# Kernel optimization log

Measured on AMD Instinct MI355X. Metric: run time of the kernel, lower is better.

## Reference

```python
import jax, jax.numpy as jnp
from jax import lax
import numpy as np

B, A, C = 8, 49104, 90
IMG = 512.0            # 512 + compound_coef*128, coef=0
SCORE_THR = 0.2
IOU_THR = 0.2
K_PRE = 1000           # top candidates kept before NMS (standard TF-style padded NMS)
K_OUT = 100            # max detections per image


def setup_inputs() -> dict:
    key = jax.random.key(0)
    k1, k2, k3, k4, k5, k6 = jax.random.split(key, 6)
    cls_preds = jax.random.uniform(k1, (B, A, C), dtype=jnp.float32)
    loc_preds = 0.1 * jax.random.normal(k2, (B, A, 4), dtype=jnp.float32)
    # plausible anchors in (y1, x1, y2, x2) within the 512x512 image
    cy = jax.random.uniform(k3, (A,)) * IMG
    cx = jax.random.uniform(k4, (A,)) * IMG
    h = 16.0 + jax.random.uniform(k5, (A,)) * 112.0
    w = 16.0 + jax.random.uniform(k6, (A,)) * 112.0
    anchors = jnp.stack([cy - h / 2, cx - w / 2, cy + h / 2, cx + w / 2], axis=-1).astype(jnp.float32)
    return {"cls_preds": cls_preds, "loc_preds": loc_preds, "anchors": anchors}


def _decode_and_clip(anchors, loc_preds):
    # anchors: [A,4] (y1,x1,y2,x2); loc_preds: [B,A,4] (dy,dx,dh,dw)
    ya = (anchors[:, 0] + anchors[:, 2]) / 2
    xa = (anchors[:, 1] + anchors[:, 3]) / 2
    ha = anchors[:, 2] - anchors[:, 0]
    wa = anchors[:, 3] - anchors[:, 1]
    dy, dx, dh, dw = loc_preds[..., 0], loc_preds[..., 1], loc_preds[..., 2], loc_preds[..., 3]
    h = jnp.exp(dh) * ha
    w = jnp.exp(dw) * wa
    yc = dy * ha + ya
    xc = dx * wa + xa
    # output boxes in (xmin, ymin, xmax, ymax), clipped to image
    boxes = jnp.stack([xc - w / 2, yc - h / 2, xc + w / 2, yc + h / 2], axis=-1)
    return jnp.clip(boxes, 0.0, IMG)


def _pairwise_iou(boxes):
    # boxes: [K,4] xyxy -> [K,K]
    x1 = jnp.maximum(boxes[:, None, 0], boxes[None, :, 0])
    y1 = jnp.maximum(boxes[:, None, 1], boxes[None, :, 1])
    x2 = jnp.minimum(boxes[:, None, 2], boxes[None, :, 2])
    y2 = jnp.minimum(boxes[:, None, 3], boxes[None, :, 3])
    inter = jnp.clip(x2 - x1, 0.0) * jnp.clip(y2 - y1, 0.0)
    area = (boxes[:, 2] - boxes[:, 0]) * (boxes[:, 3] - boxes[:, 1])
    return inter / (area[:, None] + area[None, :] - inter + 1e-8)


def _nms_single(scores, classes, boxes):
    # scores: [A], classes: [A] int32, boxes: [A,4]
    masked = jnp.where(scores > SCORE_THR, scores, -1.0)
    vals, idx = lax.top_k(masked, K_PRE)          # top candidates
    b = boxes[idx]                                 # [K_PRE,4]
    cls = classes[idx]                             # [K_PRE]
    # batched_nms trick: offset boxes per class so cross-class IoU is 0
    off = b + cls[:, None].astype(b.dtype) * (IMG + 1.0)
    ious = _pairwise_iou(off)                      # [K_PRE,K_PRE]

    def body(keep, i):
        sup = jnp.any(keep & (ious[:, i] > IOU_THR))
        k = (vals[i] > SCORE_THR) & (~sup)
        return keep.at[i].set(k), None

    keep, _ = lax.scan(body, jnp.zeros((K_PRE,), bool), jnp.arange(K_PRE))
    final = jnp.where(keep, vals, -1.0)
    fvals, fidx = lax.top_k(final, K_OUT)
    det = fvals > 0.0
    out_boxes = jnp.where(det[:, None], b[fidx], jnp.array([0.0, 0.0, 1.0, 1.0], dtype=b.dtype))
    out_scores = jnp.where(det, fvals, 0.0)
    out_labels = jnp.where(det, cls[fidx], -1)
    return out_boxes, out_scores, out_labels


def reference(cls_preds, loc_preds, anchors):
    boxes = _decode_and_clip(anchors, loc_preds)   # [B,A,4]
    scores = jnp.max(cls_preds, axis=2)            # [B,A]
    classes = jnp.argmax(cls_preds, axis=2).astype(jnp.int32)
    out_boxes, out_scores, out_labels = jax.vmap(_nms_single)(scores, classes, boxes)
    return out_boxes, out_scores, out_labels
```

## Files before the change

### kernel.cpp

```cpp
#include <hip/hip_runtime.h>
#include <stdint.h>

#define B_    8
#define A_    49104
#define C_    90
#define IMG_  512.0f
#define THR_  0.2f
#define KPRE  1000
#define KOUT  100
#define NCAND 1024
#define NKEY  2048
#define NBIN  1024
#define BINBASE 0x17C99u
#define THRU    0xBE4CCCCDu
#define GANCH 64
#define PREF_F 0.9997f

#define NPAD 1088
#define PADI(j) ((j) + ((j) >> 4))

static __device__ __forceinline__ uint32_t f2ord(float f) {
    uint32_t b = __float_as_uint(f);
    return (b & 0x80000000u) ? ~b : (b | 0x80000000u);
}
static __device__ __forceinline__ float ord2f(uint32_t u) {
    uint32_t b = (u & 0x80000000u) ? (u & 0x7FFFFFFFu) : ~u;
    return __uint_as_float(b);
}

__global__ __launch_bounds__(256)
void k_score_compact(const float* __restrict__ cls,
                     uint32_t* __restrict__ scores_u,
                     uint64_t* __restrict__ keybuf,
                     uint32_t* __restrict__ cntg) {
    __shared__ float4 s4[(GANCH * C_) / 4];
    __shared__ float r_val[GANCH];
    __shared__ int   r_cls[GANCH];

    int tid = threadIdx.x;
    int b = blockIdx.y;
    int a0 = blockIdx.x * GANCH;
    int valid = A_ - a0; if (valid > GANCH) valid = GANCH;

    const float4* src = (const float4*)(cls + (size_t)(b * A_ + a0) * C_);
    if (valid == GANCH) {
        float4 v0 = src[tid];
        float4 v1 = src[tid + 256];
        float4 v2 = src[tid + 512];
        float4 v3 = src[tid + 768];
        float4 v4 = src[tid + 1024];
        float4 v5;
        if (tid < 160) v5 = src[tid + 1280];
        s4[tid]        = v0;
        s4[tid + 256]  = v1;
        s4[tid + 512]  = v2;
        s4[tid + 768]  = v3;
        s4[tid + 1024] = v4;
        if (tid < 160) s4[tid + 1280] = v5;
    } else {
        int n4 = (valid * C_) / 4;
        for (int i = tid; i < n4; i += 256) s4[i] = src[i];
    }
    __syncthreads();

    const float* s = (const float*)s4;
    int g = tid >> 2, sub = tid & 3;
    float best = -1.0f; int bi = 0;
    if (g < valid) {
        #pragma unroll
        for (int j = sub; j < C_ + 2; j += 4) {
            if (j < C_) {
                float v = s[g * C_ + j];
                if (v > best) { best = v; bi = j; }
            }
        }
    }
    #pragma unroll
    for (int d = 1; d < 4; d <<= 1) {
        float ov = __shfl_xor(best, d);
        int   oi = __shfl_xor(bi, d);
        if (ov > best || (ov == best && oi < bi)) { best = ov; bi = oi; }
    }
    if (sub == 0 && g < valid) { r_val[g] = best; r_cls[g] = bi; }
    __syncthreads();

    if (tid < 64) {
        int a = a0 + tid;
        bool v = tid < valid;
        float bv = v ? r_val[tid] : -1.0f;
        if (v) {
            float m = (bv > THR_) ? bv : -1.0f;
            scores_u[b * A_ + a] = f2ord(m);
        }
        bool flag = v && (bv >= PREF_F);
        unsigned long long mb = __ballot(flag);
        if (mb) {
            uint32_t base = 0;
            if (tid == 0) base = atomicAdd(&cntg[b], (uint32_t)__popcll(mb));
            base = (uint32_t)__shfl((int)base, 0);
            if (flag) {
                int p = (int)base + (int)__popcll(mb & ((1ull << tid) - 1ull));
                if (p < NKEY) {
                    uint64_t key = ((uint64_t)f2ord(bv) << 32)
                                 | ((uint64_t)((~(uint32_t)a) & 0xFFFFu) << 16)
                                 | ((uint64_t)(uint32_t)r_cls[tid] << 8);
                    keybuf[b * NKEY + p] = key;
                }
            }
        }
    }
}

__global__ __launch_bounds__(1024)
void k_seltop2(const uint32_t* __restrict__ scores_u,
               const float* __restrict__ cls,
               const float* __restrict__ loc,
               const float* __restrict__ anc,
               const uint64_t* __restrict__ keybuf,
               const uint32_t* __restrict__ cntg,
               float* __restrict__ cand_val,
               int* __restrict__ cand_cls,
               float* __restrict__ cand_box,
               int* __restrict__ n_valid) {
    int b = blockIdx.x;
    int t = threadIdx.x;
    __shared__ uint64_t keys[NKEY];
    __shared__ uint32_t sh_coarse;
    __shared__ int      sh_rem;
    __shared__ uint32_t sh_cutoff;
    __shared__ int      sh_cnt;
    const uint32_t* su = scores_u + (size_t)b * A_;

    int n = (int)cntg[b];
    bool fast = (n >= KPRE && n <= NKEY);

    if (fast) {
        for (int i = t; i < NKEY; i += 1024)
            keys[i] = (i < n) ? keybuf[b * NKEY + i] : 0ull;
    } else {
        uint32_t* h = (uint32_t*)keys;
        h[t] = 0;
        if (t == 0) sh_cnt = 0;
        __syncthreads();
        for (int a = t; a < A_; a += 1024) {
            uint32_t u = su[a];
            if (u > THRU) {
                int bin = (int)(u >> 15) - (int)BINBASE;
                bin = bin < 0 ? 0 : (bin >= NBIN ? NBIN - 1 : bin);
                atomicAdd(&h[bin], 1u);
            }
        }
        __syncthreads();
        for (int d = 1; d < NBIN; d <<= 1) {
            uint32_t add = (t + d < NBIN) ? h[t + d] : 0u;
            __syncthreads();
            h[t] += add;
            __syncthreads();
        }
        {
            uint32_t St = h[t];
            uint32_t Sn = (t + 1 < NBIN) ? h[t + 1] : 0u;
            if (St >= KPRE && Sn < KPRE) {
                sh_coarse = (BINBASE + (uint32_t)t) << 15;
                sh_rem = KPRE - (int)Sn;
            }
            if (t == 0 && h[0] < KPRE) {
                sh_rem = 0;
                sh_coarse = 0xFFFFFFFFu;
                sh_cutoff = BINBASE << 15;
            }
        }
        __syncthreads();
        uint32_t coarse = sh_coarse;
        int rem = sh_rem;

        h[t] = 0;
        __syncthreads();
        if (rem > 0) {
            for (int a = t; a < A_; a += 1024) {
                uint32_t u = su[a];
                if ((u & 0xFFFF8000u) == coarse)
                    atomicAdd(&h[(u >> 5) & 0x3FF], 1u);
            }
        }
        __syncthreads();
        for (int d = 1; d < NBIN; d <<= 1) {
            uint32_t add = (t + d < NBIN) ? h[t + d] : 0u;
            __syncthreads();
            h[t] += add;
            __syncthreads();
        }
        if (rem > 0) {
            int St = (int)h[t];
            int Sn = (t + 1 < NBIN) ? (int)h[t + 1] : 0;
            if (St >= rem && Sn < rem)
                sh_cutoff = coarse | ((uint32_t)t << 5);
        }
        __syncthreads();
        uint32_t cutoff = sh_cutoff;
        __syncthreads();

        for (int a = t; a < A_; a += 1024) {
            uint32_t u = su[a];
            if (u >= cutoff) {
                int p = atomicAdd(&sh_cnt, 1);
                if (p < NKEY)
                    keys[p] = ((uint64_t)u << 32)
                            | ((uint64_t)((~(uint32_t)a) & 0xFFFFu) << 16);
            }
        }
        __syncthreads();
        n = sh_cnt; if (n > NKEY) n = NKEY;
        for (int i = t; i < NKEY; i += 1024)
            if (i >= n) keys[i] = 0ull;
    }
    __syncthreads();

    for (int kk = 2; kk <= NKEY; kk <<= 1) {
        for (int jj = kk >> 1; jj > 0; jj >>= 1) {
            int i1 = ((t & ~(jj - 1)) << 1) | (t & (jj - 1));
            int i2 = i1 + jj;
            uint64_t va = keys[i1], vb = keys[i2];
            bool desc = ((i1 & kk) == 0);
            if ((va < vb) == desc) { keys[i1] = vb; keys[i2] = va; }
            __syncthreads();
        }
    }

    uint64_t key = keys[t];
    bool real = (t < n);
    int ci = b * NCAND + t;
    if (real) {
        int a = (int)((~(uint32_t)(key >> 16)) & 0xFFFFu);
        int c;
        if (fast) {
            c = (int)((key >> 8) & 0xFFu);
        } else {
            const float* row = cls + ((size_t)b * A_ + a) * C_;
            float bb = -1.0f; int bc = 0;
            for (int j = 0; j < C_; ++j) { float q = row[j]; if (q > bb) { bb = q; bc = j; } }
            c = bc;
        }
        float4 an = ((const float4*)anc)[a];
        float4 l4 = ((const float4*)loc)[(size_t)b * A_ + a];
        float ya = (an.x + an.z) * 0.5f;
        float xa = (an.y + an.w) * 0.5f;
        float ha = an.z - an.x;
        float wa = an.w - an.y;
        float hh = expf(l4.z) * ha;
        float ww = expf(l4.w) * wa;
        float yc = l4.x * ha + ya;
        float xc = l4.y * wa + xa;
        float4 bx;
        bx.x = fminf(fmaxf(xc - ww * 0.5f, 0.0f), IMG_);
        bx.y = fminf(fmaxf(yc - hh * 0.5f, 0.0f), IMG_);
        bx.z = fminf(fmaxf(xc + ww * 0.5f, 0.0f), IMG_);
        bx.w = fminf(fmaxf(yc + hh * 0.5f, 0.0f), IMG_);
        cand_val[ci] = ord2f((uint32_t)(key >> 32));
        cand_cls[ci] = c;
        ((float4*)cand_box)[ci] = bx;
    } else {
        cand_val[ci] = -1.0f;
        cand_cls[ci] = 0;
        float4 z; z.x = z.y = z.z = z.w = 0.0f;
        ((float4*)cand_box)[ci] = z;
    }
    if (t == 0) n_valid[b] = n < KPRE ? n : KPRE;
}

__global__ void k_masks(const float* __restrict__ cand_box,
                        const int* __restrict__ cand_cls,
                        unsigned short* __restrict__ M16) {
    int b = blockIdx.x;
    __shared__ float x1s[NPAD], y1s[NPAD], x2s[NPAD], y2s[NPAD], ars[NPAD];
    for (int i = threadIdx.x; i < NCAND; i += blockDim.x) {
        int ci = b * NCAND + i;
        float4 bx = ((const float4*)cand_box)[ci];
        float off = (float)cand_cls[ci] * (IMG_ + 1.0f);
        float ox1 = bx.x + off, oy1 = bx.y + off;
        float ox2 = bx.z + off, oy2 = bx.w + off;
        int ip = PADI(i);
        x1s[ip] = ox1; y1s[ip] = oy1; x2s[ip] = ox2; y2s[ip] = oy2;
        ars[ip] = (ox2 - ox1) * (oy2 - oy1);
    }
    __syncthreads();

    int row0 = blockIdx.y * 63;
    for (int item = threadIdx.x; item < 63 * 64; item += blockDim.x) {
        int i = row0 + (item >> 6);
        if (i >= KPRE) continue;
        int w = item & 63;
        if (w < (i >> 4)) continue;
        int ip = PADI(i);
        float xi1 = x1s[ip], yi1 = y1s[ip], xi2 = x2s[ip], yi2 = y2s[ip], ai = ars[ip];
        unsigned int m = 0;
        int j0 = w * 16;
        #pragma unroll
        for (int q = 0; q < 16; ++q) {
            int jp = PADI(j0 + q);
            float xx1 = fmaxf(xi1, x1s[jp]);
            float yy1 = fmaxf(yi1, y1s[jp]);
            float xx2 = fminf(xi2, x2s[jp]);
            float yy2 = fminf(yi2, y2s[jp]);
            float iw = xx2 - xx1; iw = iw > 0.0f ? iw : 0.0f;
            float ih = yy2 - yy1; ih = ih > 0.0f ? ih : 0.0f;
            float inter = iw * ih;
            float den = (ai + ars[jp]) - inter + 1e-8f;
            float iou = inter / den;
            m |= (iou > THR_ ? 1u : 0u) << q;
        }
        M16[((size_t)(b * NCAND + i)) * 64 + w] = (unsigned short)m;
    }
}

__global__ void k_nms_out(const unsigned short* __restrict__ M16,
                          const float* __restrict__ cand_val,
                          const int* __restrict__ cand_cls,
                          const float* __restrict__ cand_box,
                          const int* __restrict__ n_valid,
                          float* __restrict__ out) {
    int b = blockIdx.x;
    int lane = threadIdx.x;
    int nv = n_valid[b]; if (nv > KPRE) nv = KPRE;
    const unsigned short* Mr = M16 + (size_t)b * NCAND * 64;
    __shared__ int kept[KOUT];

    uint32_t S = 0;
    int cnt = 0;
    uint32_t cur[8], nxt[8];
    #pragma unroll
    for (int t = 0; t < 8; ++t) cur[t] = Mr[(size_t)t * 64 + lane];

    for (int base = 0; base < nv && cnt < KOUT; base += 8) {
        #pragma unroll
        for (int t = 0; t < 8; ++t) {
            int r = base + 8 + t;
            nxt[t] = Mr[(size_t)(r < NCAND ? r : 0) * 64 + lane];
        }
        #pragma unroll
        for (int t = 0; t < 8; ++t) {
            int i = base + t;
            bool inb = (i < nv) && (cnt < KOUT);
            unsigned long long ball =
                __ballot(inb && (((S >> (i & 15)) & 1u) != 0u));
            int sup = (int)((ball >> (i >> 4)) & 1ull);
            if (inb && !sup) {
                S |= cur[t];
                if (lane == 0) kept[cnt] = i;
                cnt++;
            }
        }
        #pragma unroll
        for (int t = 0; t < 8; ++t) cur[t] = nxt[t];
    }
    __syncthreads();

    for (int s_ = lane; s_ < KOUT; s_ += 64) {
        float b0 = 0.0f, b1 = 0.0f, b2 = 1.0f, b3 = 1.0f, sc = 0.0f, lb = -1.0f;
        if (s_ < cnt) {
            int i = kept[s_];
            int ci = b * NCAND + i;
            float4 bx = ((const float4*)cand_box)[ci];
            b0 = bx.x; b1 = bx.y; b2 = bx.z; b3 = bx.w;
            sc = cand_val[ci];
            lb = (float)cand_cls[ci];
        }
        int ob = (b * KOUT + s_) * 4;
        out[ob + 0] = b0; out[ob + 1] = b1; out[ob + 2] = b2; out[ob + 3] = b3;
        out[B_ * KOUT * 4 + b * KOUT + s_] = sc;
        out[B_ * KOUT * 5 + b * KOUT + s_] = lb;
    }
}

extern "C" void kernel_launch(void* const* d_in, const int* in_sizes, int n_in,
                              void* d_out, int out_size, void* d_ws, size_t ws_size,
                              hipStream_t stream) {
    const float* cls = (const float*)d_in[0];
    const float* loc = (const float*)d_in[1];
    const float* anc = (const float*)d_in[2];
    float* out = (float*)d_out;

    char* ws = (char*)d_ws;
    size_t off = 0;
    auto alloc = [&](size_t bytes) -> void* {
        void* p = ws + off;
        off += (bytes + 255) & ~(size_t)255;
        return p;
    };
    uint32_t* scores_u = (uint32_t*)alloc((size_t)B_ * A_ * 4);
    uint64_t* keybuf   = (uint64_t*)alloc((size_t)B_ * NKEY * 8);
    uint32_t* cntg     = (uint32_t*)alloc((size_t)B_ * 4);
    float*    cand_val = (float*)   alloc((size_t)B_ * NCAND * 4);
    int*      cand_cls = (int*)     alloc((size_t)B_ * NCAND * 4);
    float*    cand_box = (float*)   alloc((size_t)B_ * NCAND * 4 * 4);
    int*      n_valid  = (int*)     alloc((size_t)B_ * 4);
    unsigned short* M16 = (unsigned short*)alloc((size_t)B_ * NCAND * 64 * 2);

    hipMemsetAsync(cntg, 0, (size_t)B_ * 4, stream);

    dim3 gD((A_ + GANCH - 1) / GANCH, B_);
    k_score_compact<<<gD, 256, 0, stream>>>(cls, scores_u, keybuf, cntg);
    k_seltop2<<<B_, 1024, 0, stream>>>(
        scores_u, cls, loc, anc, keybuf, cntg,
        cand_val, cand_cls, cand_box, n_valid);
    k_masks<<<dim3(B_, 16), 256, 0, stream>>>(cand_box, cand_cls, M16);
    k_nms_out<<<B_, 64, 0, stream>>>(
        M16, cand_val, cand_cls, cand_box, n_valid, out);
}
```

Before: 282.6 us.

## Replace global atomic compaction with per-block key slots and register bitonic sort

The score kernel no longer appends candidate keys to one global buffer through an atomic counter. Each block now writes its keys and count into its own slot, and the top-select kernel rebuilds a contiguous key array with a 1024-wide prefix scan. This removes the global atomics and the memset launch. The bitonic sort now keeps two keys per thread in registers, uses wavefront shuffles for strides below 64 and shared memory only for larger strides, so it needs fewer barriers. The cost is an extra prefix scan and serial per-block copy loops in the single-block-per-image kernel.

```diff
diff --git a/kernel.cpp b/kernel.cpp
--- a/kernel.cpp
+++ b/kernel.cpp
@@ -14,6 +14,7 @@
 #define BINBASE 0x17C99u
 #define THRU    0xBE4CCCCDu
 #define GANCH 64
+#define NBLKX ((A_ + GANCH - 1) / GANCH)
 #define PREF_F 0.9997f
 
 #define NPAD 1088
@@ -27,19 +28,26 @@
     uint32_t b = (u & 0x80000000u) ? (u & 0x7FFFFFFFu) : ~u;
     return __uint_as_float(b);
 }
+static __device__ __forceinline__ uint64_t shflx64(uint64_t v, int m) {
+    uint32_t lo = (uint32_t)v, hi = (uint32_t)(v >> 32);
+    lo = (uint32_t)__shfl_xor((int)lo, m);
+    hi = (uint32_t)__shfl_xor((int)hi, m);
+    return ((uint64_t)hi << 32) | lo;
+}
 
 __global__ __launch_bounds__(256)
 void k_score_compact(const float* __restrict__ cls,
                      uint32_t* __restrict__ scores_u,
-                     uint64_t* __restrict__ keybuf,
-                     uint32_t* __restrict__ cntg) {
+                     uint64_t* __restrict__ blk_keys,
+                     uint32_t* __restrict__ blk_cnt) {
     __shared__ float4 s4[(GANCH * C_) / 4];
     __shared__ float r_val[GANCH];
     __shared__ int   r_cls[GANCH];
 
     int tid = threadIdx.x;
     int b = blockIdx.y;
-    int a0 = blockIdx.x * GANCH;
+    int bx = blockIdx.x;
+    int a0 = bx * GANCH;
     int valid = A_ - a0; if (valid > GANCH) valid = GANCH;
 
     const float4* src = (const float4*)(cls + (size_t)(b * A_ + a0) * C_);
@@ -94,20 +102,14 @@
         }
         bool flag = v && (bv >= PREF_F);
         unsigned long long mb = __ballot(flag);
-        if (mb) {
-            uint32_t base = 0;
-            if (tid == 0) base = atomicAdd(&cntg[b], (uint32_t)__popcll(mb));
-            base = (uint32_t)__shfl((int)base, 0);
-            if (flag) {
-                int p = (int)base + (int)__popcll(mb & ((1ull << tid) - 1ull));
-                if (p < NKEY) {
-                    uint64_t key = ((uint64_t)f2ord(bv) << 32)
-                                 | ((uint64_t)((~(uint32_t)a) & 0xFFFFu) << 16)
-                                 | ((uint64_t)(uint32_t)r_cls[tid] << 8);
-                    keybuf[b * NKEY + p] = key;
-                }
-            }
-        }
+        if (flag) {
+            int pos = (int)__popcll(mb & ((1ull << tid) - 1ull));
+            uint64_t key = ((uint64_t)f2ord(bv) << 32)
+                         | ((uint64_t)((~(uint32_t)a) & 0xFFFFu) << 16)
+                         | ((uint64_t)(uint32_t)r_cls[tid] << 8);
+            blk_keys[((size_t)(b * NBLKX + bx)) * GANCH + pos] = key;
+        }
+        if (tid == 0) blk_cnt[b * NBLKX + bx] = (uint32_t)__popcll(mb);
     }
 }
 
@@ -116,8 +118,8 @@
                const float* __restrict__ cls,
                const float* __restrict__ loc,
                const float* __restrict__ anc,
-               const uint64_t* __restrict__ keybuf,
-               const uint32_t* __restrict__ cntg,
+               const uint64_t* __restrict__ blk_keys,
+               const uint32_t* __restrict__ blk_cnt,
                float* __restrict__ cand_val,
                int* __restrict__ cand_cls,
                float* __restrict__ cand_box,
@@ -125,18 +127,33 @@
     int b = blockIdx.x;
     int t = threadIdx.x;
     __shared__ uint64_t keys[NKEY];
+    __shared__ uint32_t pc[1024];
     __shared__ uint32_t sh_coarse;
     __shared__ int      sh_rem;
     __shared__ uint32_t sh_cutoff;
     __shared__ int      sh_cnt;
     const uint32_t* su = scores_u + (size_t)b * A_;
 
-    int n = (int)cntg[b];
+    uint32_t own = (t < NBLKX) ? blk_cnt[b * NBLKX + t] : 0u;
+    pc[t] = own;
+    __syncthreads();
+    for (int d = 1; d < 1024; d <<= 1) {
+        uint32_t v = (t >= d) ? pc[t - d] : 0u;
+        __syncthreads();
+        pc[t] += v;
+        __syncthreads();
+    }
+    int n = (int)pc[1023];
     bool fast = (n >= KPRE && n <= NKEY);
 
     if (fast) {
+        if (t < NBLKX && own) {
+            int base = (int)pc[t] - (int)own;
+            const uint64_t* src = blk_keys + ((size_t)(b * NBLKX + t)) * GANCH;
+            for (int j = 0; j < (int)own; ++j) keys[base + j] = src[j];
+        }
         for (int i = t; i < NKEY; i += 1024)
-            keys[i] = (i < n) ? keybuf[b * NKEY + i] : 0ull;
+            if (i >= n) keys[i] = 0ull;
     } else {
         uint32_t* h = (uint32_t*)keys;
         h[t] = 0;
@@ -216,18 +233,34 @@
     }
     __syncthreads();
 
+    uint64_t x = keys[t], y = keys[t + 1024];
     for (int kk = 2; kk <= NKEY; kk <<= 1) {
         for (int jj = kk >> 1; jj > 0; jj >>= 1) {
-            int i1 = ((t & ~(jj - 1)) << 1) | (t & (jj - 1));
-            int i2 = i1 + jj;
-            uint64_t va = keys[i1], vb = keys[i2];
-            bool desc = ((i1 & kk) == 0);
-            if ((va < vb) == desc) { keys[i1] = vb; keys[i2] = va; }
-            __syncthreads();
-        }
-    }
-
-    uint64_t key = keys[t];
+            if (jj == 1024) {
+                uint64_t mx = x > y ? x : y;
+                uint64_t mn = x > y ? y : x;
+                x = mx; y = mn;
+                continue;
+            }
+            uint64_t px, py;
+            if (jj >= 64) {
+                keys[t] = x; keys[t + 1024] = y;
+                __syncthreads();
+                px = keys[t ^ jj]; py = keys[(t + 1024) ^ jj];
+                __syncthreads();
+            } else {
+                px = shflx64(x, jj);
+                py = shflx64(y, jj);
+            }
+            bool kmx = (((t & kk) == 0) == ((t & jj) == 0));
+            x = kmx ? (x > px ? x : px) : (x > px ? px : x);
+            int ty = t + 1024;
+            bool kmy = (((ty & kk) == 0) == ((ty & jj) == 0));
+            y = kmy ? (y > py ? y : py) : (y > py ? py : y);
+        }
+    }
+
+    uint64_t key = x;
     bool real = (t < n);
     int ci = b * NCAND + t;
     if (real) {
@@ -388,20 +421,18 @@
         return p;
     };
     uint32_t* scores_u = (uint32_t*)alloc((size_t)B_ * A_ * 4);
-    uint64_t* keybuf   = (uint64_t*)alloc((size_t)B_ * NKEY * 8);
-    uint32_t* cntg     = (uint32_t*)alloc((size_t)B_ * 4);
+    uint64_t* blk_keys = (uint64_t*)alloc((size_t)B_ * NBLKX * GANCH * 8);
+    uint32_t* blk_cnt  = (uint32_t*)alloc((size_t)B_ * NBLKX * 4);
     float*    cand_val = (float*)   alloc((size_t)B_ * NCAND * 4);
     int*      cand_cls = (int*)     alloc((size_t)B_ * NCAND * 4);
     float*    cand_box = (float*)   alloc((size_t)B_ * NCAND * 4 * 4);
     int*      n_valid  = (int*)     alloc((size_t)B_ * 4);
     unsigned short* M16 = (unsigned short*)alloc((size_t)B_ * NCAND * 64 * 2);
 
-    hipMemsetAsync(cntg, 0, (size_t)B_ * 4, stream);
-
-    dim3 gD((A_ + GANCH - 1) / GANCH, B_);
-    k_score_compact<<<gD, 256, 0, stream>>>(cls, scores_u, keybuf, cntg);
+    dim3 gD(NBLKX, B_);
+    k_score_compact<<<gD, 256, 0, stream>>>(cls, scores_u, blk_keys, blk_cnt);
     k_seltop2<<<B_, 1024, 0, stream>>>(
-        scores_u, cls, loc, anc, keybuf, cntg,
+        scores_u, cls, loc, anc, blk_keys, blk_cnt,
         cand_val, cand_cls, cand_box, n_valid);
     k_masks<<<dim3(B_, 16), 256, 0, stream>>>(cand_box, cand_cls, M16);
     k_nms_out<<<B_, 64, 0, stream>>>(
```

New measurement: 269.8 us. 4.5% less time.
